# Kernel tuning notes

Hardware: AMD Instinct MI355X
Metric: run time of the kernel (lower is better)

## Reference

```python
import jax, jax.numpy as jnp
import numpy as np
import math

B, S, D, H = 2, 2048, 1024, 16
DH = D // H

def setup_inputs() -> dict:
    key0 = jax.random.key(0)
    ks = jax.random.split(key0, 12)
    s = 1.0 / math.sqrt(D)
    return {
        "query": jax.random.normal(ks[0], (B, S, D), jnp.float32),
        "key": jax.random.normal(ks[1], (B, S, D), jnp.float32),
        "value": jax.random.normal(ks[2], (B, S, D), jnp.float32),
        "mask": jax.random.randint(ks[3], (B, 1, S, S), 0, 2, jnp.int32),
        "Wq": jax.random.normal(ks[4], (D, D), jnp.float32) * s,
        "bq": jnp.zeros((D,), jnp.float32),
        "Wk": jax.random.normal(ks[5], (D, D), jnp.float32) * s,
        "bk": jnp.zeros((D,), jnp.float32),
        "Wv": jax.random.normal(ks[6], (D, D), jnp.float32) * s,
        "bv": jnp.zeros((D,), jnp.float32),
        "Wo": jax.random.normal(ks[7], (D, D), jnp.float32) * s,
        "bo": jnp.zeros((D,), jnp.float32),
    }

def reference(query, key, value, mask, Wq, bq, Wk, bk, Wv, bv, Wo, bo):
    # Linear projections (torch Linear: x @ W.T + b)
    q = query @ Wq.T + bq
    k = key @ Wk.T + bk
    v = value @ Wv.T + bv
    # [B, S, D] -> [B, H, S, DH]
    q = q.reshape(B, S, H, DH).transpose(0, 2, 1, 3)
    k = k.reshape(B, S, H, DH).transpose(0, 2, 1, 3)
    v = v.reshape(B, S, H, DH).transpose(0, 2, 1, 3)
    # scaled dot-product attention with explicit [B,H,S,S] scores
    score = jnp.einsum('bhqd,bhkd->bhqk', q, k) / math.sqrt(DH)
    score = jnp.where(mask == 0, jnp.float32(-1e9), score)
    attn = jax.nn.softmax(score, axis=-1)
    out = jnp.einsum('bhqk,bhkd->bhqd', attn, v)
    out = out.transpose(0, 2, 1, 3).reshape(B, S, D)
    return out @ Wo.T + bo
```

## Files before the change

### kernel.cpp

```cpp
#include <hip/hip_runtime.h>
#include <hip/hip_bf16.h>

typedef __attribute__((ext_vector_type(4))) float f32x4;
typedef __attribute__((ext_vector_type(8))) short bf16x8;
typedef __attribute__((ext_vector_type(4))) short s16x4;
typedef __attribute__((ext_vector_type(4))) unsigned int u32x4;
typedef unsigned short ushort_t;
typedef unsigned int u32;
typedef unsigned long long u64;

constexpr int B = 2, S = 2048, D = 1024, H = 16, DH = 64;

__device__ __forceinline__ ushort_t f2bf(float f) {
    union { float f; unsigned int i; } v; v.f = f;
    unsigned int r = v.i + 0x7fffu + ((v.i >> 16) & 1u);
    return (ushort_t)(r >> 16);
}

__device__ __forceinline__ float fast_exp2(float x) {
#if __has_builtin(__builtin_amdgcn_exp2f)
    return __builtin_amdgcn_exp2f(x);
#else
    return exp2f(x);
#endif
}

__device__ __forceinline__ u32 pack_hi16(u32 b1, u32 b0) {
#if __has_builtin(__builtin_amdgcn_perm)
    return __builtin_amdgcn_perm(b1, b0, 0x07060302u);
#else
    return (b1 & 0xffff0000u) | (b0 >> 16);
#endif
}

__device__ __forceinline__ void gload_lds16(const void* g, void* l) {
    __builtin_amdgcn_global_load_lds(
        (const __attribute__((address_space(1))) unsigned int*)g,
        (__attribute__((address_space(3))) unsigned int*)l,
        16, 0, 0);
}

__global__ __launch_bounds__(256) void cvt_f32_bf16(
    const float* __restrict__ in, ushort_t* __restrict__ out, int n)
{
    int i = (blockIdx.x * 256 + threadIdx.x) * 4;
    if (i >= n) return;
    f32x4 v = *(const f32x4*)(in + i);
    s16x4 o;
    for (int j = 0; j < 4; ++j) o[j] = (short)f2bf(v[j]);
    *(s16x4*)(out + i) = o;
}

__global__ __launch_bounds__(256) void cvt3_f32_bf16(
    const float* __restrict__ a0, const float* __restrict__ a1,
    const float* __restrict__ a2, ushort_t* __restrict__ out, int n)
{
    const float* in = blockIdx.y == 0 ? a0 : (blockIdx.y == 1 ? a1 : a2);
    int i = (blockIdx.x * 256 + threadIdx.x) * 4;
    if (i >= n) return;
    f32x4 v = *(const f32x4*)(in + i);
    s16x4 o;
    for (int j = 0; j < 4; ++j) o[j] = (short)f2bf(v[j]);
    *(s16x4*)(out + (size_t)blockIdx.y * n + i) = o;
}

__global__ __launch_bounds__(256) void cvt4_f32_bf16(
    const float* __restrict__ a0, const float* __restrict__ a1,
    const float* __restrict__ a2, const float* __restrict__ a3,
    ushort_t* __restrict__ out, int n)
{
    const float* in = blockIdx.y == 0 ? a0 : (blockIdx.y == 1 ? a1 :
                      (blockIdx.y == 2 ? a2 : a3));
    int i = (blockIdx.x * 256 + threadIdx.x) * 4;
    if (i >= n) return;
    f32x4 v = *(const f32x4*)(in + i);
    s16x4 o;
    for (int j = 0; j < 4; ++j) o[j] = (short)f2bf(v[j]);
    *(s16x4*)(out + (size_t)blockIdx.y * n + i) = o;
}

__global__ __launch_bounds__(256) void pack_mask(
    const int* __restrict__ mask, u64* __restrict__ pm)
{
    const int wave_g = (blockIdx.x * 256 + threadIdx.x) >> 6;
    const int lane = threadIdx.x & 63;
    for (int w = 0; w < 16; ++w) {
        size_t idx = (size_t)wave_g * 16 + w;
        int mv = mask[idx * 64 + lane];
        u64 bal = __ballot(mv != 0);
        if (lane == 0) {
            int t = (int)(idx & 31);
            int q = (int)((idx >> 5) & (S - 1));
            int b = (int)(idx >> 16);
            pm[((size_t)b * 32 + t) * S + q] = bal;
        }
    }
}

__global__ __launch_bounds__(256) void transpose_v(
    const ushort_t* __restrict__ Vw, ushort_t* __restrict__ Vt)
{
    __shared__ ushort_t T[64][80];
    const int st = blockIdx.x, bh = blockIdx.y;
    const int b = bh / H, h = bh % H;
    const int tid = threadIdx.x;
    const int r = tid >> 3, c = tid & 7;
    for (int p = 0; p < 2; ++p) {
        int s = p * 32 + r;
        bf16x8 v = *(const bf16x8*)(Vw + (size_t)(b * S + st * 64 + s) * D + h * DH + c * 8);
        *(bf16x8*)(&T[s][c * 8]) = v;
    }
    __syncthreads();
    const int q0q = (c >> 2) * 8 + (c & 3);
    for (int p = 0; p < 2; ++p) {
        int d = p * 32 + r;
        bf16x8 o;
        for (int j = 0; j < 4; ++j) o[j]     = (short)T[q0q * 4 + j][d];
        for (int j = 0; j < 4; ++j) o[4 + j] = (short)T[(q0q + 4) * 4 + j][d];
        *(bf16x8*)(Vt + (size_t)((b * H + h) * DH + d) * S + st * 64 + c * 8) = o;
    }
}

template <typename OutT>
__device__ __forceinline__ void gemm_body128(
    const ushort_t* __restrict__ Ag,
    const ushort_t* __restrict__ Wg,
    const float* __restrict__ bias,
    OutT* __restrict__ Cg,
    ushort_t* __restrict__ VtOut,
    int M, int N, int K,
    ushort_t* SH, bool vepi)
{
    constexpr int BK = 64;
    ushort_t* As = SH;
    ushort_t* Bs = SH + 128 * 64;
    const int tid  = threadIdx.x;
    const int wid  = tid >> 6;
    const int lane = tid & 63;
    const int m0 = blockIdx.x * 128;
    const int n0 = blockIdx.y * 128;
    const int wr = wid >> 1, wc = wid & 1;

    const int lrow = lane & 15;
    const int lk8  = (lane >> 4) * 8;
    const int srow  = lane >> 3;
    const int sbyte = (lane & 7) * 16;

    f32x4 acc[4][4] = {};

    for (int k0 = 0; k0 < K; k0 += BK) {
        #pragma unroll
        for (int c = 0; c < 4; ++c) {
            int r0 = wid * 32 + c * 8;
            gload_lds16((const char*)(Ag + (size_t)(m0 + r0 + srow) * K + k0) + sbyte,
                        (char*)As + r0 * 128);
            gload_lds16((const char*)(Wg + (size_t)(n0 + r0 + srow) * K + k0) + sbyte,
                        (char*)Bs + r0 * 128);
        }
        __syncthreads();

        #pragma unroll
        for (int kk = 0; kk < BK; kk += 32) {
            bf16x8 af[4], bfr[4];
            #pragma unroll
            for (int i = 0; i < 4; ++i) {
                af[i]  = *(const bf16x8*)(As + (wr * 64 + i * 16 + lrow) * BK + kk + lk8);
                bfr[i] = *(const bf16x8*)(Bs + (wc * 64 + i * 16 + lrow) * BK + kk + lk8);
            }
            #pragma unroll
            for (int i = 0; i < 4; ++i)
                #pragma unroll
                for (int j = 0; j < 4; ++j)
                    acc[i][j] = __builtin_amdgcn_mfma_f32_16x16x32_bf16(
                        af[i], bfr[j], acc[i][j], 0, 0, 0);
        }
        __syncthreads();
    }

    const int hi    = lane >> 4;
    const int crow0 = hi * 4;
    const int ccol  = lane & 15;

    if (vepi) {
        #pragma unroll
        for (int j = 0; j < 4; ++j) {
            int dl = wc * 64 + j * 16 + ccol;
            float bv = bias[n0 + dl];
            #pragma unroll
            for (int i = 0; i < 4; ++i) {
                int pos = wr * 64 + ((i >> 1) * 4 + hi) * 8 + (i & 1) * 4;
                s16x4 o;
                #pragma unroll
                for (int r = 0; r < 4; ++r) o[r] = (short)f2bf(acc[i][j][r] + bv);
                *(s16x4*)(SH + dl * 132 + pos) = o;
            }
        }
        __syncthreads();
        const int b = m0 >> 11;
        const int sbase = m0 & (S - 1);
        #pragma unroll
        for (int rr = 0; rr < 32; ++rr) {
            int dl = wid * 32 + rr;
            int dg = n0 + dl;
            u32 w2 = *(const u32*)(SH + dl * 132 + lane * 2);
            *(u32*)(VtOut + ((size_t)(b * H + (dg >> 6)) * DH + (dg & 63)) * S
                    + sbase + lane * 2) = w2;
        }
    } else {
        #pragma unroll
        for (int j = 0; j < 4; ++j) {
            int col = n0 + wc * 64 + j * 16 + ccol;
            float bv = bias[col];
            #pragma unroll
            for (int i = 0; i < 4; ++i) {
                #pragma unroll
                for (int r = 0; r < 4; ++r) {
                    int row = m0 + wr * 64 + i * 16 + crow0 + r;
                    float val = acc[i][j][r] + bv;
                    if constexpr (__is_same(OutT, float))
                        Cg[(size_t)row * N + col] = val;
                    else
                        Cg[(size_t)row * N + col] = f2bf(val);
                }
            }
        }
    }
}

template <typename OutT>
__device__ __forceinline__ void gemm_body64(
    const ushort_t* __restrict__ Ag,
    const ushort_t* __restrict__ Wg,
    const float* __restrict__ bias,
    OutT* __restrict__ Cg,
    int M, int N, int K,
    ushort_t* As, ushort_t* Bs)
{
    constexpr int BK = 64;
    const int tid  = threadIdx.x;
    const int wid  = tid >> 6;
    const int lane = tid & 63;
    const int m0 = blockIdx.x * 128;
    const int n0 = blockIdx.y * 64;
    const int wr = wid >> 1, wc = wid & 1;

    const int lrow = lane & 15;
    const int lk8  = (lane >> 4) * 8;
    const int srow  = lane >> 3;
    const int sbyte = (lane & 7) * 16;

    f32x4 acc[4][2] = {};

    for (int k0 = 0; k0 < K; k0 += BK) {
        #pragma unroll
        for (int c = 0; c < 4; ++c) {
            int r0 = wid * 32 + c * 8;
            gload_lds16((const char*)(Ag + (size_t)(m0 + r0 + srow) * K + k0) + sbyte,
                        (char*)As + r0 * 128);
        }
        #pragma unroll
        for (int c = 0; c < 2; ++c) {
            int r0 = wid * 16 + c * 8;
            gload_lds16((const char*)(Wg + (size_t)(n0 + r0 + srow) * K + k0) + sbyte,
                        (char*)Bs + r0 * 128);
        }
        __syncthreads();

        #pragma unroll
        for (int kk = 0; kk < BK; kk += 32) {
            bf16x8 af[4], bfr[2];
            #pragma unroll
            for (int i = 0; i < 4; ++i)
                af[i]  = *(const bf16x8*)(As + (wr * 64 + i * 16 + lrow) * BK + kk + lk8);
            #pragma unroll
            for (int j = 0; j < 2; ++j)
                bfr[j] = *(const bf16x8*)(Bs + (wc * 32 + j * 16 + lrow) * BK + kk + lk8);
            #pragma unroll
            for (int i = 0; i < 4; ++i)
                #pragma unroll
                for (int j = 0; j < 2; ++j)
                    acc[i][j] = __builtin_amdgcn_mfma_f32_16x16x32_bf16(
                        af[i], bfr[j], acc[i][j], 0, 0, 0);
        }
        __syncthreads();
    }

    const int crow0 = (lane >> 4) * 4;
    const int ccol  = lane & 15;
    #pragma unroll
    for (int j = 0; j < 2; ++j) {
        int col = n0 + wc * 32 + j * 16 + ccol;
        float bv = bias[col];
        #pragma unroll
        for (int i = 0; i < 4; ++i) {
            #pragma unroll
            for (int r = 0; r < 4; ++r) {
                int row = m0 + wr * 64 + i * 16 + crow0 + r;
                float val = acc[i][j][r] + bv;
                if constexpr (__is_same(OutT, float))
                    Cg[(size_t)row * N + col] = val;
                else
                    Cg[(size_t)row * N + col] = f2bf(val);
            }
        }
    }
}

template <typename OutT>
__global__ __launch_bounds__(256, 4) void gemm_bt_bias(
    const ushort_t* __restrict__ Ag, const ushort_t* __restrict__ Wg,
    const float* __restrict__ bias, OutT* __restrict__ Cg,
    int M, int N, int K)
{
    __shared__ ushort_t As[128 * 64];
    __shared__ ushort_t Bs[64 * 64];
    gemm_body64<OutT>(Ag, Wg, bias, Cg, M, N, K, As, Bs);
}

__global__ __launch_bounds__(256, 2) void gemm_qkv(
    const ushort_t* __restrict__ X3,
    const ushort_t* __restrict__ W4,
    const float* __restrict__ b0, const float* __restrict__ b1,
    const float* __restrict__ b2,
    ushort_t* __restrict__ QKV,
    ushort_t* __restrict__ Vt,
    int M, int N, int K)
{
    __shared__ ushort_t SH[128 * 132];
    const int z = blockIdx.z;
    const float* bias = z == 0 ? b0 : (z == 1 ? b1 : b2);
    gemm_body128<ushort_t>(X3 + (size_t)z * M * K, W4 + (size_t)z * N * K,
                           bias, QKV + (size_t)z * M * N, Vt,
                           M, N, K, SH, z == 2);
}

__global__ __launch_bounds__(256, 4) void attn_kernel(
    const ushort_t* __restrict__ Q,
    const ushort_t* __restrict__ Kt,
    const ushort_t* __restrict__ Vt,
    const u64* __restrict__ pmask,
    ushort_t* __restrict__ O)
{
    constexpr int NT2 = S / 128;
    constexpr float C1 = 0.18033688f;
    constexpr float C2 = 17.31234049f;
    __shared__ ushort_t Ks[2][64 * DH];
    __shared__ ushort_t Vs[2][64 * DH];

    const int tid  = threadIdx.x;
    const int wid  = tid >> 6;
    const int lane = tid & 63;
    const int qt = blockIdx.x;
    const int bh = blockIdx.y;
    const int b = bh / H, h = bh % H;
    const int q0 = qt * 64 + wid * 16;

    const int lq   = lane & 15;
    const int hi   = lane >> 4;
    const int lk8  = hi * 8;
    const int srow = lane >> 3;
    const int sbyte = (((lane & 7) ^ srow) & 7) * 16;

    bf16x8 qf[2];
    #pragma unroll
    for (int kk = 0; kk < 2; ++kk)
        qf[kk] = *(const bf16x8*)(Q + (size_t)(b * S + q0 + lq) * D + h * DH + kk * 32 + lk8);

    f32x4 oacc[4] = {};
    f32x4 ps = {};
    const u32x4 onesw = {0x3f803f80u, 0x3f803f80u, 0x3f803f80u, 0x3f803f80u};
    const bf16x8 onesf = __builtin_bit_cast(bf16x8, onesw);

    const u64* pmrow = pmask + (size_t)b * 32 * S + q0 + lq;
    const ushort_t* Vtb = Vt + (size_t)(b * H + h) * DH * S;

    auto compute = [&](const ushort_t* Kc, const ushort_t* Vc, u64 mw) {
        f32x4 sc[4] = {};
        #pragma unroll
        for (int kk = 0; kk < 2; ++kk) {
            const int chunk = ((kk * 4 + hi) ^ (lq & 7)) * 8;
            #pragma unroll
            for (int ni = 0; ni < 4; ++ni) {
                bf16x8 kf = *(const bf16x8*)(Kc + (ni * 16 + lq) * 64 + chunk);
                sc[ni] = __builtin_amdgcn_mfma_f32_16x16x32_bf16(kf, qf[kk], sc[ni], 0, 0, 0);
            }
        }
        const u32 lo32 = (u32)mw;
        const u32 hi32 = (u32)(mw >> 32);
        u32 paw[8];
        #pragma unroll
        for (int ni = 0; ni < 4; ++ni) {
            const u32 word = (ni < 2) ? lo32 : hi32;
            const int base = (ni & 1) * 16 + hi * 4;
            u32 pb[4];
            #pragma unroll
            for (int r = 0; r < 4; ++r) {
                float p = fast_exp2(__builtin_fmaf(sc[ni][r], C1, -C2));
                int mbit = ((int)(word << (31 - (base + r)))) >> 31;
                pb[r] = __builtin_bit_cast(u32, p) & (u32)mbit;
            }
            paw[ni * 2]     = pack_hi16(pb[1], pb[0]);
            paw[ni * 2 + 1] = pack_hi16(pb[3], pb[2]);
        }
        #pragma unroll
        for (int kk = 0; kk < 2; ++kk) {
            u32x4 pv = {paw[kk * 4], paw[kk * 4 + 1], paw[kk * 4 + 2], paw[kk * 4 + 3]};
            bf16x8 paf = __builtin_bit_cast(bf16x8, pv);
            ps = __builtin_amdgcn_mfma_f32_16x16x32_bf16(paf, onesf, ps, 0, 0, 0);
            const int chunk = ((kk * 4 + hi) ^ (lq & 7)) * 8;
            #pragma unroll
            for (int di = 0; di < 4; ++di) {
                bf16x8 vf = *(const bf16x8*)(Vc + (di * 16 + lq) * 64 + chunk);
                oacc[di] = __builtin_amdgcn_mfma_f32_16x16x32_bf16(paf, vf, oacc[di], 0, 0, 0);
            }
        }
    };

    for (int t = 0; t < NT2; ++t) {
        #pragma unroll
        for (int half = 0; half < 2; ++half) {
            const int kv0 = (t * 2 + half) * 64;
            #pragma unroll
            for (int c = 0; c < 2; ++c) {
                int r0 = wid * 16 + c * 8;
                gload_lds16((const char*)(Kt + (size_t)(b * S + kv0 + r0 + srow) * D + h * DH) + sbyte,
                            (char*)Ks[half] + r0 * 128);
                gload_lds16((const char*)(Vtb + (size_t)(r0 + srow) * S + kv0) + sbyte,
                            (char*)Vs[half] + r0 * 128);
            }
        }
        const u64 mwa = pmrow[(size_t)(t * 2) * S];
        const u64 mwb = pmrow[(size_t)(t * 2 + 1) * S];
        __syncthreads();

        compute(Ks[0], Vs[0], mwa);
        compute(Ks[1], Vs[1], mwb);
        __syncthreads();
    }

    float inv[4];
    #pragma unroll
    for (int r = 0; r < 4; ++r) inv[r] = 1.0f / ps[r];
    #pragma unroll
    for (int di = 0; di < 4; ++di) {
        #pragma unroll
        for (int r = 0; r < 4; ++r) {
            float v = oacc[di][r] * inv[r];
            O[(size_t)(b * S + q0 + hi * 4 + r) * D + h * DH + di * 16 + lq] = f2bf(v);
        }
    }
}

extern "C" void kernel_launch(void* const* d_in, const int* in_sizes, int n_in,
                              void* d_out, int out_size, void* d_ws, size_t ws_size,
                              hipStream_t stream) {
    const float* query = (const float*)d_in[0];
    const float* key   = (const float*)d_in[1];
    const float* value = (const float*)d_in[2];
    const int*   mask  = (const int*)d_in[3];
    const float* Wq = (const float*)d_in[4];
    const float* bq = (const float*)d_in[5];
    const float* Wk = (const float*)d_in[6];
    const float* bk = (const float*)d_in[7];
    const float* Wv = (const float*)d_in[8];
    const float* bv = (const float*)d_in[9];
    const float* Wo = (const float*)d_in[10];
    const float* bo = (const float*)d_in[11];
    float* out = (float*)d_out;

    const int M = B * S;
    const int NX = M * D;
    const int NW = D * D;

    char* ws = (char*)d_ws;
    const size_t MB = 1024 * 1024;
    dim3 gblk64(M / 128, D / 64);
    const int gcX = NX / (4 * 256);
    const int gcW = NW / (4 * 256);
    const int pmBlocks = (B * S * (S / 64)) / (16 * 4);

    if (ws_size >= 58 * MB) {
        ushort_t* X3  = (ushort_t*)(ws);
        ushort_t* Ow  = (ushort_t*)(ws + 8 * MB);
        ushort_t* W4  = (ushort_t*)(ws + 24 * MB);
        ushort_t* QKV = (ushort_t*)(ws + 32 * MB);
        ushort_t* Qw = QKV, *Kw = QKV + NX;
        ushort_t* Vtb = QKV + 2 * (size_t)NX;
        u64* pm = (u64*)(ws + 56 * MB);

        cvt3_f32_bf16<<<dim3(gcX, 3), 256, 0, stream>>>(query, key, value, X3, NX);
        cvt4_f32_bf16<<<dim3(gcW, 4), 256, 0, stream>>>(Wq, Wk, Wv, Wo, W4, NW);
        pack_mask<<<pmBlocks, 256, 0, stream>>>(mask, pm);

        gemm_qkv<<<dim3(M / 128, D / 128, 3), 256, 0, stream>>>(
            X3, W4, bq, bk, bv, QKV, Vtb, M, D, D);

        attn_kernel<<<dim3(S / 64, B * H), 256, 0, stream>>>(Qw, Kw, Vtb, pm, Ow);

        gemm_bt_bias<float><<<gblk64, 256, 0, stream>>>(Ow, W4 + 3 * (size_t)NW, bo, out, M, D, D);
    } else {
        ushort_t* Xb = (ushort_t*)(ws);
        ushort_t* Vtb = (ushort_t*)(ws);
        ushort_t* Wb = (ushort_t*)(ws + 8  * MB);
        u64*      pm = (u64*)(ws + 8 * MB);
        ushort_t* Qw = (ushort_t*)(ws + 16 * MB);
        ushort_t* Kw = (ushort_t*)(ws + 24 * MB);
        ushort_t* Vw = (ushort_t*)(ws + 32 * MB);
        ushort_t* Ow = (ushort_t*)(ws + 40 * MB);

        cvt_f32_bf16<<<gcX, 256, 0, stream>>>(query, Xb, NX);
        cvt_f32_bf16<<<gcW, 256, 0, stream>>>(Wq, Wb, NW);
        gemm_bt_bias<ushort_t><<<gblk64, 256, 0, stream>>>(Xb, Wb, bq, Qw, M, D, D);

        cvt_f32_bf16<<<gcX, 256, 0, stream>>>(key, Xb, NX);
        cvt_f32_bf16<<<gcW, 256, 0, stream>>>(Wk, Wb, NW);
        gemm_bt_bias<ushort_t><<<gblk64, 256, 0, stream>>>(Xb, Wb, bk, Kw, M, D, D);

        cvt_f32_bf16<<<gcX, 256, 0, stream>>>(value, Xb, NX);
        cvt_f32_bf16<<<gcW, 256, 0, stream>>>(Wv, Wb, NW);
        gemm_bt_bias<ushort_t><<<gblk64, 256, 0, stream>>>(Xb, Wb, bv, Vw, M, D, D);

        transpose_v<<<dim3(S / 64, B * H), 256, 0, stream>>>(Vw, Vtb);
        pack_mask<<<pmBlocks, 256, 0, stream>>>(mask, pm);

        attn_kernel<<<dim3(S / 64, B * H), 256, 0, stream>>>(Qw, Kw, Vtb, pm, Ow);

        cvt_f32_bf16<<<gcW, 256, 0, stream>>>(Wo, Wb, NW);
        gemm_bt_bias<float><<<gblk64, 256, 0, stream>>>(Ow, Wb, bo, out, M, D, D);
    }
}
```

Baseline: 139.5 us.

## Merge conversion and mask-pack kernels into one launch; remap attention block order

Replaces the separate activation conversion, weight conversion and mask packing kernels with a single prep_all launch that dispatches work by blockIdx.y. This cuts kernel launch overhead and gaps between small kernels. The attention kernel also remaps its linear block id so that consecutive blocks spread across (batch, head) pairs, which can change L2 and XCD locality. The merged grid includes idle blocks for the weight and mask rows, which exit early.

```diff
diff --git a/kernel.cpp b/kernel.cpp
--- a/kernel.cpp
+++ b/kernel.cpp
@@ -51,32 +51,53 @@
     *(s16x4*)(out + i) = o;
 }
 
-__global__ __launch_bounds__(256) void cvt3_f32_bf16(
-    const float* __restrict__ a0, const float* __restrict__ a1,
-    const float* __restrict__ a2, ushort_t* __restrict__ out, int n)
-{
-    const float* in = blockIdx.y == 0 ? a0 : (blockIdx.y == 1 ? a1 : a2);
-    int i = (blockIdx.x * 256 + threadIdx.x) * 4;
-    if (i >= n) return;
-    f32x4 v = *(const f32x4*)(in + i);
-    s16x4 o;
-    for (int j = 0; j < 4; ++j) o[j] = (short)f2bf(v[j]);
-    *(s16x4*)(out + (size_t)blockIdx.y * n + i) = o;
-}
-
-__global__ __launch_bounds__(256) void cvt4_f32_bf16(
-    const float* __restrict__ a0, const float* __restrict__ a1,
-    const float* __restrict__ a2, const float* __restrict__ a3,
-    ushort_t* __restrict__ out, int n)
-{
-    const float* in = blockIdx.y == 0 ? a0 : (blockIdx.y == 1 ? a1 :
-                      (blockIdx.y == 2 ? a2 : a3));
-    int i = (blockIdx.x * 256 + threadIdx.x) * 4;
-    if (i >= n) return;
-    f32x4 v = *(const f32x4*)(in + i);
-    s16x4 o;
-    for (int j = 0; j < 4; ++j) o[j] = (short)f2bf(v[j]);
-    *(s16x4*)(out + (size_t)blockIdx.y * n + i) = o;
+__global__ __launch_bounds__(256) void prep_all(
+    const float* __restrict__ qin, const float* __restrict__ kin,
+    const float* __restrict__ vin,
+    const float* __restrict__ wq, const float* __restrict__ wk,
+    const float* __restrict__ wv, const float* __restrict__ wo,
+    const int* __restrict__ mask,
+    ushort_t* __restrict__ X3, ushort_t* __restrict__ W4,
+    u64* __restrict__ pm, int nx, int nw)
+{
+    const int y = blockIdx.y;
+    if (y < 3) {
+        const float* in = y == 0 ? qin : (y == 1 ? kin : vin);
+        int i = (blockIdx.x * 256 + threadIdx.x) * 4;
+        if (i >= nx) return;
+        f32x4 v = *(const f32x4*)(in + i);
+        s16x4 o;
+        #pragma unroll
+        for (int j = 0; j < 4; ++j) o[j] = (short)f2bf(v[j]);
+        *(s16x4*)(X3 + (size_t)y * nx + i) = o;
+    } else if (y == 3) {
+        int wsel = blockIdx.x >> 10;
+        int xb = blockIdx.x & 1023;
+        const float* in = wsel == 0 ? wq : (wsel == 1 ? wk :
+                          (wsel == 2 ? wv : wo));
+        int i = (xb * 256 + threadIdx.x) * 4;
+        if (i >= nw) return;
+        f32x4 v = *(const f32x4*)(in + i);
+        s16x4 o;
+        #pragma unroll
+        for (int j = 0; j < 4; ++j) o[j] = (short)f2bf(v[j]);
+        *(s16x4*)(W4 + (size_t)wsel * nw + i) = o;
+    } else {
+        if (blockIdx.x >= 2048) return;
+        const int wave_g = (blockIdx.x * 256 + threadIdx.x) >> 6;
+        const int lane = threadIdx.x & 63;
+        for (int w = 0; w < 16; ++w) {
+            size_t idx = (size_t)wave_g * 16 + w;
+            int mv = mask[idx * 64 + lane];
+            u64 bal = __ballot(mv != 0);
+            if (lane == 0) {
+                int t = (int)(idx & 31);
+                int q = (int)((idx >> 5) & (S - 1));
+                int b = (int)(idx >> 16);
+                pm[((size_t)b * 32 + t) * S + q] = bal;
+            }
+        }
+    }
 }
 
 __global__ __launch_bounds__(256) void pack_mask(
@@ -350,8 +371,10 @@
     const int tid  = threadIdx.x;
     const int wid  = tid >> 6;
     const int lane = tid & 63;
-    const int qt = blockIdx.x;
-    const int bh = blockIdx.y;
+    const int bid = blockIdx.x + 32 * blockIdx.y;
+    const int j8  = bid >> 3;
+    const int bh  = (bid & 7) * 4 + (j8 >> 5);
+    const int qt  = j8 & 31;
     const int b = bh / H, h = bh % H;
     const int q0 = qt * 64 + wid * 16;
 
@@ -488,9 +511,8 @@
         ushort_t* Vtb = QKV + 2 * (size_t)NX;
         u64* pm = (u64*)(ws + 56 * MB);
 
-        cvt3_f32_bf16<<<dim3(gcX, 3), 256, 0, stream>>>(query, key, value, X3, NX);
-        cvt4_f32_bf16<<<dim3(gcW, 4), 256, 0, stream>>>(Wq, Wk, Wv, Wo, W4, NW);
-        pack_mask<<<pmBlocks, 256, 0, stream>>>(mask, pm);
+        prep_all<<<dim3(gcX, 5), 256, 0, stream>>>(
+            query, key, value, Wq, Wk, Wv, Wo, mask, X3, W4, pm, NX, NW);
 
         gemm_qkv<<<dim3(M / 128, D / 128, 3), 256, 0, stream>>>(
             X3, W4, bq, bk, bv, QKV, Vtb, M, D, D);
```

Result: faster. 135.3 us (-3.0%).
